# Performance work log

Measured on AMD Instinct MI355X. Metric: run time of the kernel, lower is better.

## Reference

```python
import jax, jax.numpy as jnp
import numpy as np


def _sobel_filters():
    # 3D Sobel kernels for x, y, z directions, shape (3, 1, 3, 3, 3) in OIDHW.
    x = np.array([[[-1, 0, 1], [-2, 0, 2], [-1, 0, 1]],
                  [[-2, 0, 2], [-4, 0, 4], [-2, 0, 2]],
                  [[-1, 0, 1], [-2, 0, 2], [-1, 0, 1]]], dtype=np.float32)
    y = np.array([[[1, 2, 1], [0, 0, 0], [-1, -2, -1]],
                  [[2, 4, 2], [0, 0, 0], [-2, -4, -2]],
                  [[1, 2, 1], [0, 0, 0], [-1, -2, -1]]], dtype=np.float32)
    z = np.array([[[1, 2, 1], [2, 4, 2], [1, 2, 1]],
                  [[0, 0, 0], [0, 0, 0], [0, 0, 0]],
                  [[-1, -2, -1], [-2, -4, -2], [-1, -2, -1]]], dtype=np.float32)
    return jnp.asarray(np.stack([x, y, z])[:, None])  # (3,1,3,3,3)


_FILTERS = _sobel_filters()
_EPS = 1e-10


def gradient3d(x):
    # x: [B,1,D,H,W] -> gradient magnitude [B,1,D,H,W].
    # Single conv with 3 output channels == three separate torch conv3d + concat.
    g = jax.lax.conv_general_dilated(
        x, _FILTERS, window_strides=(1, 1, 1),
        padding=[(1, 1), (1, 1), (1, 1)],
        dimension_numbers=('NCDHW', 'OIDHW', 'NCDHW'))  # [B,3,D,H,W]
    return jnp.sqrt(jnp.sum(g * g, axis=1, keepdims=True) + _EPS)


def setup_inputs() -> dict:
    key = jax.random.key(0)
    k1, k2, k3 = jax.random.split(key, 3)
    shape = (2, 1, 192, 192, 192)
    pred = jax.random.normal(k1, shape, dtype=jnp.float32)
    gt_dose = jax.random.normal(k2, shape, dtype=jnp.float32)
    body_mask = (jax.random.uniform(k3, shape) > 0.3).astype(jnp.float32)
    return {"pred": pred, "gt_dose": gt_dose, "body_mask": body_mask}


def reference(pred, gt_dose, body_mask):
    mse = jnp.square(pred - gt_dose) * body_mask
    mge = jnp.square(gradient3d(gt_dose) - gradient3d(pred)) * body_mask
    return jnp.mean(mse + jnp.tanh(mge) * mse)
```

## Files before the change

### kernel.cpp

```cpp
#include <hip/hip_runtime.h>
#include <math.h>

#define W 192
#define H 192
#define DEPTH 192
#define BATCH 2
#define TW 64
#define TH 8
#define DC 12
#define HW (H * W)
#define VOL ((size_t)DEPTH * HW)
#define NPL (DC + 2)
#define GX ((W / TW) * (H / TH))
#define GY (DEPTH / DC)
#define NBLK (GX * GY * BATCH)

__global__ __launch_bounds__(256) void sobel_loss_part(
    const float* __restrict__ pred, const float* __restrict__ gt,
    const float* __restrict__ mask, float* __restrict__ partials)
{
    const int tid = threadIdx.x;
    const int tx = blockIdx.x % 3;
    const int ty = blockIdx.x / 3;
    const int w0 = tx * TW, h0 = ty * TH;
    const int d0 = blockIdx.y * DC;
    const size_t base = (size_t)blockIdx.z * VOL;

    const int wv  = tid >> 6;
    const int col = tid & 63;
    const int colg = w0 + col;
    const int ra = h0 + 2 * wv;

    int yoff[4]; float rmask[4];
    #pragma unroll
    for (int r = 0; r < 4; ++r) {
        int y = ra - 1 + r;
        rmask[r] = ((unsigned)y < (unsigned)H) ? 1.f : 0.f;
        int yc = y < 0 ? 0 : (y > H - 1 ? H - 1 : y);
        yoff[r] = yc * W;
    }
    const float lmk = (colg > 0)     ? 1.f : 0.f;
    const float rmk = (colg < W - 1) ? 1.f : 0.f;
    const int cl = colg > 0     ? colg - 1 : 0;
    const int cr = colg < W - 1 ? colg + 1 : W - 1;

    const float* __restrict__ A0 = pred + base;
    const float* __restrict__ A1 = gt + base;
    const float* __restrict__ MB = mask + base + (size_t)ra * W + colg;

    float dx[2][2][3], dy[2][2][3], sm[2][2][3], ct[2][2][2];
    #pragma unroll
    for (int a = 0; a < 2; ++a)
        #pragma unroll
        for (int o = 0; o < 2; ++o) {
            dx[a][o][0]=dx[a][o][1]=dx[a][o][2]=0.f;
            dy[a][o][0]=dy[a][o][1]=dy[a][o][2]=0.f;
            sm[a][o][0]=sm[a][o][1]=sm[a][o][2]=0.f;
            ct[a][o][0]=ct[a][o][1]=0.f;
        }
    float acc = 0.f;
    float2 Mc = make_float2(0.f, 0.f), Mn = make_float2(0.f, 0.f);

    #pragma unroll
    for (int i = 0; i < NPL; ++i) {
        const int p = d0 - 1 + i;
        const float pm = ((unsigned)p < (unsigned)DEPTH) ? 1.f : 0.f;
        const int  pc = p < 0 ? 0 : (p > DEPTH - 1 ? DEPTH - 1 : p);
        const size_t pb = (size_t)pc * HW;

        if (i >= 1 && i <= DC) {
            const float* mp = MB + (size_t)p * HW;
            Mn = make_float2(mp[0], mp[W]);
        }

        float msk[4];
        #pragma unroll
        for (int r = 0; r < 4; ++r) msk[r] = rmask[r] * pm;

        float rs[2][4], rd[2][4], cc[2][2];
        #pragma unroll
        for (int a = 0; a < 2; ++a) {
            const float* src = (a ? A1 : A0) + pb;
            #pragma unroll
            for (int r = 0; r < 4; ++r) {
                const float* rp = src + yoff[r];
                float m = rp[colg];
                float l = rp[cl] * lmk;
                float q = rp[cr] * rmk;
                rs[a][r] = msk[r] * (l + 2.f * m + q);
                rd[a][r] = msk[r] * (q - l);
                if (r == 1) cc[a][0] = msk[r] * m;
                if (r == 2) cc[a][1] = msk[r] * m;
            }
        }

        #pragma unroll
        for (int a = 0; a < 2; ++a)
            #pragma unroll
            for (int o = 0; o < 2; ++o) {
                dx[a][o][0] = dx[a][o][1]; dx[a][o][1] = dx[a][o][2];
                dx[a][o][2] = rd[a][o] + 2.f * rd[a][o+1] + rd[a][o+2];
                sm[a][o][0] = sm[a][o][1]; sm[a][o][1] = sm[a][o][2];
                sm[a][o][2] = rs[a][o] + 2.f * rs[a][o+1] + rs[a][o+2];
                dy[a][o][0] = dy[a][o][1]; dy[a][o][1] = dy[a][o][2];
                dy[a][o][2] = rs[a][o] - rs[a][o+2];
                ct[a][o][0] = ct[a][o][1]; ct[a][o][1] = cc[a][o];
            }

        if (i >= 2) {
            const float2 M = Mc;
            #pragma unroll
            for (int o = 0; o < 2; ++o) {
                float gxa = dx[0][o][0] + 2.f * dx[0][o][1] + dx[0][o][2];
                float gya = dy[0][o][0] + 2.f * dy[0][o][1] + dy[0][o][2];
                float gza = sm[0][o][0] - sm[0][o][2];
                float gxb = dx[1][o][0] + 2.f * dx[1][o][1] + dx[1][o][2];
                float gyb = dy[1][o][0] + 2.f * dy[1][o][1] + dy[1][o][2];
                float gzb = sm[1][o][0] - sm[1][o][2];
                float ga = __builtin_amdgcn_sqrtf(gxa * gxa + gya * gya + gza * gza + 1e-10f);
                float gb = __builtin_amdgcn_sqrtf(gxb * gxb + gyb * gyb + gzb * gzb + 1e-10f);
                float m  = o ? M.y : M.x;
                float dm = ct[0][o][0] - ct[1][o][0];
                float mse = dm * dm * m;
                float dg  = gb - ga;
                float mge = dg * dg * m;
                float ex = __expf(2.f * mge);
                float t  = 1.f - 2.f * __builtin_amdgcn_rcpf(ex + 1.f);
                acc += mse * (1.f + t);
            }
        }
        Mc = Mn;
    }

    float v = acc;
    #pragma unroll
    for (int o = 32; o > 0; o >>= 1) v += __shfl_down(v, o, 64);
    __shared__ float red[4];
    if ((tid & 63) == 0) red[tid >> 6] = v;
    __syncthreads();
    if (tid == 0) {
        partials[(size_t)blockIdx.z * (GX * GY)
                 + (size_t)blockIdx.y * GX + blockIdx.x]
            = red[0] + red[1] + red[2] + red[3];
    }
}

__global__ __launch_bounds__(256) void reduce_final(
    const float* __restrict__ partials, int n, float* __restrict__ out)
{
    int tid = threadIdx.x;
    double s = 0.0;
    for (int i = tid; i < n; i += 256) s += (double)partials[i];
    #pragma unroll
    for (int o = 32; o > 0; o >>= 1) s += __shfl_down(s, o, 64);
    __shared__ double red[4];
    if ((tid & 63) == 0) red[tid >> 6] = s;
    __syncthreads();
    if (tid == 0) {
        double t = red[0] + red[1] + red[2] + red[3];
        const double ntot = (double)BATCH * (double)DEPTH * (double)H * (double)W;
        out[0] = (float)(t / ntot);
    }
}

extern "C" void kernel_launch(void* const* d_in, const int* in_sizes, int n_in,
                              void* d_out, int out_size, void* d_ws, size_t ws_size,
                              hipStream_t stream) {
    const float* pred = (const float*)d_in[0];
    const float* gt   = (const float*)d_in[1];
    const float* mask = (const float*)d_in[2];
    float* partials = (float*)d_ws;

    dim3 grid(GX, GY, BATCH);
    sobel_loss_part<<<grid, 256, 0, stream>>>(pred, gt, mask, partials);

    reduce_final<<<1, 256, 0, stream>>>(partials, NBLK, (float*)d_out);
}
```

Before: 189.4 us.

## Stage input planes in LDS via double-buffered direct global-to-LDS loads

```diff
diff --git a/kernel.cpp b/kernel.cpp
--- a/kernel.cpp
+++ b/kernel.cpp
@@ -5,48 +5,83 @@
 #define H 192
 #define DEPTH 192
 #define BATCH 2
-#define TW 64
 #define TH 8
 #define DC 12
+#define NT 768
 #define HW (H * W)
 #define VOL ((size_t)DEPTH * HW)
 #define NPL (DC + 2)
-#define GX ((W / TW) * (H / TH))
+#define SROWS 10
+#define SITEMS 960
+#define BUFFLOATS 3840
+#define GX (H / TH)
 #define GY (DEPTH / DC)
 #define NBLK (GX * GY * BATCH)
 
-__global__ __launch_bounds__(256) void sobel_loss_part(
+__device__ __align__(16) float g_zero16[16] = {0.f};
+
+__global__ __launch_bounds__(NT) void sobel_loss_part(
     const float* __restrict__ pred, const float* __restrict__ gt,
     const float* __restrict__ mask, float* __restrict__ partials)
 {
+    __shared__ __align__(16) float lds[2 * BUFFLOATS];
+    __shared__ float red[12];
+
     const int tid = threadIdx.x;
-    const int tx = blockIdx.x % 3;
-    const int ty = blockIdx.x / 3;
-    const int w0 = tx * TW, h0 = ty * TH;
+    const int ty = blockIdx.x;
+    const int h0 = ty * TH;
     const int d0 = blockIdx.y * DC;
     const size_t base = (size_t)blockIdx.z * VOL;
 
-    const int wv  = tid >> 6;
-    const int col = tid & 63;
-    const int colg = w0 + col;
-    const int ra = h0 + 2 * wv;
-
-    int yoff[4]; float rmask[4];
-    #pragma unroll
-    for (int r = 0; r < 4; ++r) {
-        int y = ra - 1 + r;
-        rmask[r] = ((unsigned)y < (unsigned)H) ? 1.f : 0.f;
-        int yc = y < 0 ? 0 : (y > H - 1 ? H - 1 : y);
-        yoff[r] = yc * W;
-    }
-    const float lmk = (colg > 0)     ? 1.f : 0.f;
-    const float rmk = (colg < W - 1) ? 1.f : 0.f;
-    const int cl = colg > 0     ? colg - 1 : 0;
-    const int cr = colg < W - 1 ? colg + 1 : W - 1;
-
-    const float* __restrict__ A0 = pred + base;
-    const float* __restrict__ A1 = gt + base;
-    const float* __restrict__ MB = mask + base + (size_t)ra * W + colg;
+    const int wvi  = tid >> 6;
+    const int lane = tid & 63;
+    const int pr   = wvi / 3;
+    const int cg   = wvi % 3;
+    const int col  = cg * 64 + lane;
+
+    const int   dl  = (col > 0) ? 1 : 0;
+    const int   dr  = (col < W - 1) ? 1 : 0;
+    const float lmk = (col > 0) ? 1.f : 0.f;
+    const float rmk = (col < W - 1) ? 1.f : 0.f;
+
+    int it_act[2], it_ok[2];
+    size_t it_goff[2];
+    const float* it_src[2];
+    #pragma unroll
+    for (int k = 0; k < 2; ++k) {
+        int j = tid + NT * k;
+        int act = (j < SITEMS);
+        int jj = act ? j : 0;
+        int a = jj / 480; int e = jj - a * 480;
+        int r = e / 48;   int c = e - r * 48;
+        int y = h0 - 1 + r;
+        int rowok = ((unsigned)y < (unsigned)H);
+        it_act[k]  = act;
+        it_ok[k]   = act && rowok;
+        it_goff[k] = it_ok[k] ? ((size_t)y * W + 4 * c) : 0;
+        it_src[k]  = a ? gt : pred;
+    }
+
+    typedef const __attribute__((address_space(1))) void GV;
+    typedef __attribute__((address_space(3))) void LV;
+
+    auto dma_plane = [&](int i) {
+        const int p = d0 - 1 + i;
+        const bool pv = ((unsigned)p < (unsigned)DEPTH);
+        float* bufp = lds + (i & 1) * BUFFLOATS;
+        #pragma unroll
+        for (int k = 0; k < 2; ++k) {
+            if (it_act[k]) {
+                const float* ga = (pv && it_ok[k])
+                    ? (it_src[k] + base + (size_t)p * HW + it_goff[k]) : g_zero16;
+                __builtin_amdgcn_global_load_lds((GV*)ga,
+                    (LV*)(bufp + (wvi << 8) + k * 3072), 16, 0, 0);
+            }
+        }
+    };
+
+    const float* MB = mask + base + (size_t)(h0 + 2 * pr) * W + col;
+    float2 Mn = make_float2(0.f, 0.f), Mc;
 
     float dx[2][2][3], dy[2][2][3], sm[2][2][3], ct[2][2][2];
     #pragma unroll
@@ -59,38 +94,37 @@
             ct[a][o][0]=ct[a][o][1]=0.f;
         }
     float acc = 0.f;
-    float2 Mc = make_float2(0.f, 0.f), Mn = make_float2(0.f, 0.f);
-
-    #pragma unroll
+
+    dma_plane(0);
+
     for (int i = 0; i < NPL; ++i) {
-        const int p = d0 - 1 + i;
-        const float pm = ((unsigned)p < (unsigned)DEPTH) ? 1.f : 0.f;
-        const int  pc = p < 0 ? 0 : (p > DEPTH - 1 ? DEPTH - 1 : p);
-        const size_t pb = (size_t)pc * HW;
-
-        if (i >= 1 && i <= DC) {
-            const float* mp = MB + (size_t)p * HW;
-            Mn = make_float2(mp[0], mp[W]);
-        }
-
-        float msk[4];
-        #pragma unroll
-        for (int r = 0; r < 4; ++r) msk[r] = rmask[r] * pm;
+        asm volatile("s_waitcnt vmcnt(0)" ::: "memory");
+        __builtin_amdgcn_sched_barrier(0);
+        __builtin_amdgcn_s_barrier();
+        __builtin_amdgcn_sched_barrier(0);
+
+        Mc = Mn;
+        if (i + 1 < NPL) dma_plane(i + 1);
+        if (i >= 1 && i <= DC)
+            Mn = make_float2(MB[(size_t)(d0 + i - 1) * HW],
+                             MB[(size_t)(d0 + i - 1) * HW + W]);
+
+        const float* buf = lds + (i & 1) * BUFFLOATS;
 
         float rs[2][4], rd[2][4], cc[2][2];
         #pragma unroll
         for (int a = 0; a < 2; ++a) {
-            const float* src = (a ? A1 : A0) + pb;
+            const int ab = a * 1920 + (2 * pr) * 192 + col;
             #pragma unroll
-            for (int r = 0; r < 4; ++r) {
-                const float* rp = src + yoff[r];
-                float m = rp[colg];
-                float l = rp[cl] * lmk;
-                float q = rp[cr] * rmk;
-                rs[a][r] = msk[r] * (l + 2.f * m + q);
-                rd[a][r] = msk[r] * (q - l);
-                if (r == 1) cc[a][0] = msk[r] * m;
-                if (r == 2) cc[a][1] = msk[r] * m;
+            for (int rr = 0; rr < 4; ++rr) {
+                const int o = ab + rr * 192;
+                float m = buf[o];
+                float l = buf[o - dl] * lmk;
+                float r = buf[o + dr] * rmk;
+                rs[a][rr] = l + 2.f * m + r;
+                rd[a][rr] = r - l;
+                if (rr == 1) cc[a][0] = m;
+                if (rr == 2) cc[a][1] = m;
             }
         }
 
@@ -129,19 +163,19 @@
                 acc += mse * (1.f + t);
             }
         }
-        Mc = Mn;
     }
 
     float v = acc;
     #pragma unroll
     for (int o = 32; o > 0; o >>= 1) v += __shfl_down(v, o, 64);
-    __shared__ float red[4];
     if ((tid & 63) == 0) red[tid >> 6] = v;
     __syncthreads();
     if (tid == 0) {
+        float bs = 0.f;
+        #pragma unroll
+        for (int iw = 0; iw < 12; ++iw) bs += red[iw];
         partials[(size_t)blockIdx.z * (GX * GY)
-                 + (size_t)blockIdx.y * GX + blockIdx.x]
-            = red[0] + red[1] + red[2] + red[3];
+                 + (size_t)blockIdx.y * GX + blockIdx.x] = bs;
     }
 }
 
@@ -172,7 +206,7 @@
     float* partials = (float*)d_ws;
 
     dim3 grid(GX, GY, BATCH);
-    sobel_loss_part<<<grid, 256, 0, stream>>>(pred, gt, mask, partials);
+    sobel_loss_part<<<grid, NT, 0, stream>>>(pred, gt, mask, partials);
 
     reduce_final<<<1, 256, 0, stream>>>(partials, NBLK, (float*)d_out);
 }
```

New measurement: 201.2 us. 6.3% more time.

## Stage input planes in LDS via async global_load_lds double buffering

Applied to the files above, without the earlier changes.

```diff
diff --git a/kernel.cpp b/kernel.cpp
--- a/kernel.cpp
+++ b/kernel.cpp
@@ -6,19 +6,29 @@
 #define DEPTH 192
 #define BATCH 2
 #define TW 64
-#define TH 8
+#define TH 16
 #define DC 12
 #define HW (H * W)
 #define VOL ((size_t)DEPTH * HW)
 #define NPL (DC + 2)
+#define LROW 72
+#define LROWS 18
+#define LPLANE (LROW * LROWS)
+#define NITEM 648
+#define BUFFLOATS 2592
 #define GX ((W / TW) * (H / TH))
 #define GY (DEPTH / DC)
 #define NBLK (GX * GY * BATCH)
+
+__device__ __align__(16) float g_zero16[16] = {0.f};
 
 __global__ __launch_bounds__(256) void sobel_loss_part(
     const float* __restrict__ pred, const float* __restrict__ gt,
     const float* __restrict__ mask, float* __restrict__ partials)
 {
+    __shared__ __align__(16) float lds[2 * BUFFLOATS];
+    __shared__ float red[4];
+
     const int tid = threadIdx.x;
     const int tx = blockIdx.x % 3;
     const int ty = blockIdx.x / 3;
@@ -26,116 +36,142 @@
     const int d0 = blockIdx.y * DC;
     const size_t base = (size_t)blockIdx.z * VOL;
 
-    const int wv  = tid >> 6;
-    const int col = tid & 63;
-    const int colg = w0 + col;
-    const int ra = h0 + 2 * wv;
-
-    int yoff[4]; float rmask[4];
-    #pragma unroll
-    for (int r = 0; r < 4; ++r) {
-        int y = ra - 1 + r;
-        rmask[r] = ((unsigned)y < (unsigned)H) ? 1.f : 0.f;
-        int yc = y < 0 ? 0 : (y > H - 1 ? H - 1 : y);
-        yoff[r] = yc * W;
-    }
-    const float lmk = (colg > 0)     ? 1.f : 0.f;
-    const float rmk = (colg < W - 1) ? 1.f : 0.f;
-    const int cl = colg > 0     ? colg - 1 : 0;
-    const int cr = colg < W - 1 ? colg + 1 : W - 1;
-
-    const float* __restrict__ A0 = pred + base;
-    const float* __restrict__ A1 = gt + base;
-    const float* __restrict__ MB = mask + base + (size_t)ra * W + colg;
-
-    float dx[2][2][3], dy[2][2][3], sm[2][2][3], ct[2][2][2];
-    #pragma unroll
-    for (int a = 0; a < 2; ++a)
-        #pragma unroll
-        for (int o = 0; o < 2; ++o) {
-            dx[a][o][0]=dx[a][o][1]=dx[a][o][2]=0.f;
-            dy[a][o][0]=dy[a][o][1]=dy[a][o][2]=0.f;
-            sm[a][o][0]=sm[a][o][1]=sm[a][o][2]=0.f;
-            ct[a][o][0]=ct[a][o][1]=0.f;
-        }
-    float acc = 0.f;
-    float2 Mc = make_float2(0.f, 0.f), Mn = make_float2(0.f, 0.f);
-
-    #pragma unroll
-    for (int i = 0; i < NPL; ++i) {
+    const int rp = tid >> 5;
+    const int cp = tid & 31;
+    const int t0 = 2 * rp;
+    const int c0 = 2 * cp;
+
+    int it_act[3], it_ok[3];
+    size_t it_goff[3];
+    const float* it_src[3];
+    #pragma unroll
+    for (int k = 0; k < 3; ++k) {
+        int j = tid + 256 * k;
+        int act = (j < NITEM);
+        int jj = act ? j : 0;
+        int a = jj / 324; int e = jj - a * 324;
+        int r = e / 18;   int c = e - r * 18;
+        int y  = h0 - 1 + r;
+        int xf = w0 - 4 + 4 * c;
+        it_act[k] = act;
+        it_ok[k]  = act && ((unsigned)y < (unsigned)H) && ((unsigned)xf < (unsigned)W);
+        it_goff[k] = it_ok[k] ? ((size_t)y * W + xf) : 0;
+        it_src[k]  = (jj >= 324) ? gt : pred;
+    }
+
+    typedef const __attribute__((address_space(1))) void GV;
+    typedef __attribute__((address_space(3))) void LV;
+
+    auto dma_plane = [&](int i) {
         const int p = d0 - 1 + i;
-        const float pm = ((unsigned)p < (unsigned)DEPTH) ? 1.f : 0.f;
-        const int  pc = p < 0 ? 0 : (p > DEPTH - 1 ? DEPTH - 1 : p);
-        const size_t pb = (size_t)pc * HW;
-
-        if (i >= 1 && i <= DC) {
-            const float* mp = MB + (size_t)p * HW;
-            Mn = make_float2(mp[0], mp[W]);
-        }
-
-        float msk[4];
-        #pragma unroll
-        for (int r = 0; r < 4; ++r) msk[r] = rmask[r] * pm;
-
-        float rs[2][4], rd[2][4], cc[2][2];
-        #pragma unroll
-        for (int a = 0; a < 2; ++a) {
-            const float* src = (a ? A1 : A0) + pb;
-            #pragma unroll
-            for (int r = 0; r < 4; ++r) {
-                const float* rp = src + yoff[r];
-                float m = rp[colg];
-                float l = rp[cl] * lmk;
-                float q = rp[cr] * rmk;
-                rs[a][r] = msk[r] * (l + 2.f * m + q);
-                rd[a][r] = msk[r] * (q - l);
-                if (r == 1) cc[a][0] = msk[r] * m;
-                if (r == 2) cc[a][1] = msk[r] * m;
+        const bool pv = ((unsigned)p < (unsigned)DEPTH);
+        float* bufp = lds + (i & 1) * BUFFLOATS;
+        #pragma unroll
+        for (int k = 0; k < 3; ++k) {
+            if (it_act[k]) {
+                const float* ga = (pv && it_ok[k])
+                    ? (it_src[k] + base + (size_t)p * HW + it_goff[k]) : g_zero16;
+                __builtin_amdgcn_global_load_lds((GV*)ga,
+                    (LV*)(bufp + ((tid >> 6) << 8) + (k << 10)), 16, 0, 0);
             }
         }
-
+    };
+
+    float X[2][2][2][3], S[2][2][2][3], Y[2][2][2][3], C[2][2][2][2];
+    #pragma unroll
+    for (int a = 0; a < 2; ++a)
+        #pragma unroll
+        for (int o = 0; o < 2; ++o)
+            #pragma unroll
+            for (int u = 0; u < 2; ++u) {
+                X[a][o][u][0]=X[a][o][u][1]=X[a][o][u][2]=0.f;
+                S[a][o][u][0]=S[a][o][u][1]=S[a][o][u][2]=0.f;
+                Y[a][o][u][0]=Y[a][o][u][1]=Y[a][o][u][2]=0.f;
+                C[a][o][u][0]=C[a][o][u][1]=0.f;
+            }
+    float acc = 0.f;
+    float2 Mc[2], Mn[2];
+    Mc[0]=Mc[1]=Mn[0]=Mn[1]=make_float2(0.f,0.f);
+
+    const float* MB = mask + base + (size_t)(h0 + t0) * W + (w0 + c0);
+
+    dma_plane(0);
+
+    #pragma unroll
+    for (int i = 0; i < NPL; ++i) {
+        asm volatile("s_waitcnt vmcnt(0)" ::: "memory");
+        __builtin_amdgcn_sched_barrier(0);
+        __builtin_amdgcn_s_barrier();
+        __builtin_amdgcn_sched_barrier(0);
+
+        if (i + 1 < NPL) dma_plane(i + 1);
+
+        Mc[0] = Mn[0]; Mc[1] = Mn[1];
+        if (i >= 1 && i <= DC) {
+            const float* mp = MB + (size_t)(d0 + i - 1) * HW;
+            Mn[0] = *(const float2*)mp;
+            Mn[1] = *(const float2*)(mp + W);
+        }
+
+        const float* buf = lds + (i & 1) * BUFFLOATS;
+
+        float hs[2][4][2], hd[2][4][2], cen[2][2][2];
         #pragma unroll
         for (int a = 0; a < 2; ++a)
             #pragma unroll
-            for (int o = 0; o < 2; ++o) {
-                dx[a][o][0] = dx[a][o][1]; dx[a][o][1] = dx[a][o][2];
-                dx[a][o][2] = rd[a][o] + 2.f * rd[a][o+1] + rd[a][o+2];
-                sm[a][o][0] = sm[a][o][1]; sm[a][o][1] = sm[a][o][2];
-                sm[a][o][2] = rs[a][o] + 2.f * rs[a][o+1] + rs[a][o+2];
-                dy[a][o][0] = dy[a][o][1]; dy[a][o][1] = dy[a][o][2];
-                dy[a][o][2] = rs[a][o] - rs[a][o+2];
-                ct[a][o][0] = ct[a][o][1]; ct[a][o][1] = cc[a][o];
+            for (int rr = 0; rr < 4; ++rr) {
+                const float* bp = buf + a * LPLANE + (t0 + rr) * LROW + (c0 + 3);
+                float f0 = bp[0], f1 = bp[1], f2 = bp[2], f3 = bp[3];
+                hs[a][rr][0] = f0 + 2.f * f1 + f2;
+                hs[a][rr][1] = f1 + 2.f * f2 + f3;
+                hd[a][rr][0] = f2 - f0;
+                hd[a][rr][1] = f3 - f1;
+                if (rr == 1) { cen[a][0][0] = f1; cen[a][0][1] = f2; }
+                if (rr == 2) { cen[a][1][0] = f1; cen[a][1][1] = f2; }
             }
 
+        const int ai = i % 3, a1 = (i + 2) % 3, a2 = (i + 1) % 3;
+        const int ci = i & 1, cm = (i + 1) & 1;
+        #pragma unroll
+        for (int a = 0; a < 2; ++a)
+            #pragma unroll
+            for (int o = 0; o < 2; ++o)
+                #pragma unroll
+                for (int u = 0; u < 2; ++u) {
+                    X[a][o][u][ai] = hd[a][o][u] + 2.f * hd[a][o+1][u] + hd[a][o+2][u];
+                    S[a][o][u][ai] = hs[a][o][u] + 2.f * hs[a][o+1][u] + hs[a][o+2][u];
+                    Y[a][o][u][ai] = hs[a][o][u] - hs[a][o+2][u];
+                    C[a][o][u][ci] = cen[a][o][u];
+                }
+
         if (i >= 2) {
-            const float2 M = Mc;
-            #pragma unroll
-            for (int o = 0; o < 2; ++o) {
-                float gxa = dx[0][o][0] + 2.f * dx[0][o][1] + dx[0][o][2];
-                float gya = dy[0][o][0] + 2.f * dy[0][o][1] + dy[0][o][2];
-                float gza = sm[0][o][0] - sm[0][o][2];
-                float gxb = dx[1][o][0] + 2.f * dx[1][o][1] + dx[1][o][2];
-                float gyb = dy[1][o][0] + 2.f * dy[1][o][1] + dy[1][o][2];
-                float gzb = sm[1][o][0] - sm[1][o][2];
-                float ga = __builtin_amdgcn_sqrtf(gxa * gxa + gya * gya + gza * gza + 1e-10f);
-                float gb = __builtin_amdgcn_sqrtf(gxb * gxb + gyb * gyb + gzb * gzb + 1e-10f);
-                float m  = o ? M.y : M.x;
-                float dm = ct[0][o][0] - ct[1][o][0];
-                float mse = dm * dm * m;
-                float dg  = gb - ga;
-                float mge = dg * dg * m;
-                float ex = __expf(2.f * mge);
-                float t  = 1.f - 2.f * __builtin_amdgcn_rcpf(ex + 1.f);
-                acc += mse * (1.f + t);
-            }
+            #pragma unroll
+            for (int o = 0; o < 2; ++o)
+                #pragma unroll
+                for (int u = 0; u < 2; ++u) {
+                    float gxa = X[0][o][u][a2] + 2.f * X[0][o][u][a1] + X[0][o][u][ai];
+                    float gya = Y[0][o][u][a2] + 2.f * Y[0][o][u][a1] + Y[0][o][u][ai];
+                    float gza = S[0][o][u][a2] - S[0][o][u][ai];
+                    float gxb = X[1][o][u][a2] + 2.f * X[1][o][u][a1] + X[1][o][u][ai];
+                    float gyb = Y[1][o][u][a2] + 2.f * Y[1][o][u][a1] + Y[1][o][u][ai];
+                    float gzb = S[1][o][u][a2] - S[1][o][u][ai];
+                    float ga = __builtin_amdgcn_sqrtf(gxa*gxa + gya*gya + gza*gza + 1e-10f);
+                    float gb = __builtin_amdgcn_sqrtf(gxb*gxb + gyb*gyb + gzb*gzb + 1e-10f);
+                    float m  = u ? Mc[o].y : Mc[o].x;
+                    float dm = C[0][o][u][cm] - C[1][o][u][cm];
+                    float mse = dm * dm * m;
+                    float dg  = gb - ga;
+                    float mge = dg * dg * m;
+                    float ex = __expf(2.f * mge);
+                    float t  = 1.f - 2.f * __builtin_amdgcn_rcpf(ex + 1.f);
+                    acc += mse * (1.f + t);
+                }
         }
-        Mc = Mn;
     }
 
     float v = acc;
     #pragma unroll
     for (int o = 32; o > 0; o >>= 1) v += __shfl_down(v, o, 64);
-    __shared__ float red[4];
     if ((tid & 63) == 0) red[tid >> 6] = v;
     __syncthreads();
     if (tid == 0) {
```

After: 229.0 us. 1.21x slower.
